# Performance work log

Hardware: AMD Instinct MI355X
Metric: run time of the kernel (lower is better)

## Reference

```python
import jax, jax.numpy as jnp
import numpy as np

B, S, D = 4, 2048, 1024
E, H = 1024, 16
HD = E // H
TEMPERATURE = 1.0


def setup_inputs() -> dict:
    key = jax.random.key(0)
    ks = jax.random.split(key, 6)
    x = jax.random.normal(ks[0], (B, S, D), dtype=jnp.float32)
    src_key_padding_mask = jnp.zeros((B, S), dtype=bool)  # unused by module
    matrix_mask = jax.random.normal(ks[1], (B, S, S), dtype=jnp.float32)
    # Xavier-uniform linear weights (torch Linear stores [out, in])
    lim_qkv = float(np.sqrt(6.0 / (D + 3 * E)))
    qkv_w = jax.random.uniform(ks[2], (3 * E, D), dtype=jnp.float32, minval=-lim_qkv, maxval=lim_qkv)
    qkv_b = jnp.zeros((3 * E,), dtype=jnp.float32)
    lim_o = float(np.sqrt(6.0 / (E + E)))
    o_w = jax.random.uniform(ks[3], (E, E), dtype=jnp.float32, minval=-lim_o, maxval=lim_o)
    o_b = jnp.zeros((E,), dtype=jnp.float32)
    return {"x": x, "src_key_padding_mask": src_key_padding_mask, "matrix_mask": matrix_mask,
            "qkv_w": qkv_w, "qkv_b": qkv_b, "o_w": o_w, "o_b": o_b}


def reference(x, src_key_padding_mask, matrix_mask, qkv_w, qkv_b, o_w, o_b):
    b, s, _ = x.shape
    qkv = x @ qkv_w.T + qkv_b                      # [B,S,3E]
    qkv = qkv.reshape(b, s, H, 3 * HD).transpose(0, 2, 1, 3)  # [B,H,S,3*HD]
    q, k, v = jnp.split(qkv, 3, axis=-1)           # each [B,H,S,HD]
    scale = 1.0 / np.sqrt(HD)
    logits = jnp.einsum('bhqd,bhkd->bhqk', q, k) * scale + matrix_mask[:, None, :, :]
    attn = jax.nn.softmax(logits / TEMPERATURE, axis=-1)  # [B,H,S,S]
    # dropout=0.0, eval mode -> no-op
    values = jnp.einsum('bhqk,bhkd->bhqd', attn, v)       # [B,H,S,HD]
    values = values.transpose(0, 2, 1, 3).reshape(b, s, E)
    o = values @ o_w.T + o_b                       # [B,S,E]
    attention_mean = jnp.mean(attn, axis=1)        # [B,S,S]
    return (o, attention_mean)
```

## Files before the change

### kernel.cpp

```cpp
#include <hip/hip_runtime.h>

#define B_ 4
#define S_ 2048
#define D_ 1024
#define E_ 1024
#define H_ 16
#define HD_ 64
#define SCALE 0.125f
#define LOG2E 1.44269504f
#define C1_ (SCALE * LOG2E)

typedef __bf16 bf16;
typedef __bf16 bf16x8 __attribute__((ext_vector_type(8)));
typedef __bf16 bf16x4 __attribute__((ext_vector_type(4)));
typedef float f32x4 __attribute__((ext_vector_type(4)));
typedef _Float16 f16x8 __attribute__((ext_vector_type(8)));
typedef _Float16 f16x4 __attribute__((ext_vector_type(4)));

static __device__ __forceinline__ f32x4 mfma16(bf16x8 a, bf16x8 b, f32x4 c) {
  return __builtin_amdgcn_mfma_f32_16x16x32_bf16(a, b, c, 0, 0, 0);
}

typedef __attribute__((address_space(3))) void lvoid;
typedef const __attribute__((address_space(1))) void gvoid;
static __device__ __forceinline__ void gload16(const void* g, void* l) {
  __builtin_amdgcn_global_load_lds((gvoid*)g, (lvoid*)l, 16, 0, 0);
}

static __device__ __forceinline__ float exp2a(float x) {
  float r;
  asm("v_exp_f32 %0, %1" : "=v"(r) : "v"(x));
  return r;
}

static __device__ __forceinline__ int rsw(int row) {
  return (row & 3) | (((row >> 3) & 1) << 2);
}

__global__ void k_cvt(const float* __restrict__ in, bf16* __restrict__ out, int n4) {
  int i = blockIdx.x * 256 + threadIdx.x;
  if (i >= n4) return;
  float4 v = reinterpret_cast<const float4*>(in)[i];
  bf16x4 o = { (bf16)v.x, (bf16)v.y, (bf16)v.z, (bf16)v.w };
  reinterpret_cast<bf16x4*>(out)[i] = o;
}

__global__ void k_cvt16(const float* __restrict__ in, _Float16* __restrict__ out, int n4) {
  int i = blockIdx.x * 256 + threadIdx.x;
  if (i >= n4) return;
  float4 v = reinterpret_cast<const float4*>(in)[i];
  f16x4 o = { (_Float16)(v.x * LOG2E), (_Float16)(v.y * LOG2E),
              (_Float16)(v.z * LOG2E), (_Float16)(v.w * LOG2E) };
  reinterpret_cast<f16x4*>(out)[i] = o;
}

__global__ __launch_bounds__(256) void k_qkv(const bf16* __restrict__ xb,
                                             const bf16* __restrict__ wb,
                                             const float* __restrict__ qkvb,
                                             bf16* __restrict__ Qw,
                                             bf16* __restrict__ Kw,
                                             bf16* __restrict__ Vtw) {
  __shared__ __align__(16) bf16 lA[128 * 32];
  __shared__ __align__(16) bf16 lB[128 * 32];
  const int tid = threadIdx.x, lane = tid & 63, wv = tid >> 6;
  const int u = lane >> 4, c = lane & 15;
  const int wr = wv >> 1, wc = wv & 1;
  const int m0 = blockIdx.y * 128;
  const int n0 = blockIdx.x * 128;
  const int sr = tid >> 2, sk = (tid & 3) * 8;
  const bf16* gA = xb + (size_t)(m0 + sr) * D_ + sk;
  const bf16* gB = wb + (size_t)(n0 + sr) * D_ + sk;
  bf16* lpA = lA + wv * 512;
  bf16* lpB = lB + wv * 512;
  f32x4 acc[4][4] = {};
  for (int k0 = 0; k0 < D_; k0 += 32) {
    gload16(gA + k0, lpA);
    gload16(gA + 64 * D_ + k0, lpA + 2048);
    gload16(gB + k0, lpB);
    gload16(gB + 64 * D_ + k0, lpB + 2048);
    __syncthreads();
    bf16x8 af[4], bfr[4];
#pragma unroll
    for (int m = 0; m < 4; ++m)
      af[m] = *(const bf16x8*)(lA + (wr * 64 + m * 16 + c) * 32 + u * 8);
#pragma unroll
    for (int n = 0; n < 4; ++n)
      bfr[n] = *(const bf16x8*)(lB + (wc * 64 + n * 16 + c) * 32 + u * 8);
#pragma unroll
    for (int m = 0; m < 4; ++m)
#pragma unroll
      for (int n = 0; n < 4; ++n)
        acc[m][n] = mfma16(af[m], bfr[n], acc[m][n]);
    __syncthreads();
  }
#pragma unroll
  for (int n = 0; n < 4; ++n) {
    int nn = n0 + wc * 64 + n * 16 + c;
    float bias = qkvb[nn];
    int h = nn / 192;
    int rem = nn - h * 192;
#pragma unroll
    for (int m = 0; m < 4; ++m) {
#pragma unroll
      for (int r = 0; r < 4; ++r) {
        int q = m0 + wr * 64 + m * 16 + 4 * u + r;
        int bb = q >> 11, s = q & 2047;
        bf16 v = (bf16)(acc[m][n][r] + bias);
        if (rem < 64)       Qw[((bb * H_ + h) * S_ + s) * HD_ + rem] = v;
        else if (rem < 128) Kw[((bb * H_ + h) * S_ + s) * HD_ + (rem - 64)] = v;
        else                Vtw[((bb * H_ + h) * HD_ + (rem - 128)) * S_ + s] = v;
      }
    }
  }
}

#define PV_TILE2(HC, HN, BS, KT, PF)                                          \
  {                                                                           \
    if (PF) {                                                                 \
      const bf16* ksrc = Kb + (size_t)((KT) + 1) * 64 * HD_;                  \
      gload16(ksrc + ksw1, (bf16*)kl[(BS) ^ 1] + wv * 512);                   \
      gload16(ksrc + ksw2, (bf16*)kl[(BS) ^ 1] + 2048 + wv * 512);            \
      const bf16* vsrc = Vb + (size_t)((KT) + 1) * 64;                        \
      gload16(vsrc + vsw1, (bf16*)vl[(BS) ^ 1] + wv * 512);                   \
      gload16(vsrc + vsw2, (bf16*)vl[(BS) ^ 1] + 2048 + wv * 512);            \
      __builtin_amdgcn_sched_barrier(0);                                      \
    }                                                                         \
    f32x4 sA[4], sB[4];                                                       \
    _Pragma("unroll")                                                         \
    for (int f = 0; f < 4; ++f) {                                             \
      int rk = 32 * (f & 1) + 8 * (c >> 2) + 4 * (f >> 1) + (c & 3);          \
      int sw = rsw(rk);                                                       \
      bf16x8 k0 = *(const bf16x8*)&kl[BS][rk * 64 + ((u ^ sw) * 8)];          \
      bf16x8 k1 = *(const bf16x8*)&kl[BS][rk * 64 + (((4 + u) ^ sw) * 8)];    \
      f32x4 a = {};                                                           \
      a = mfma16(k0, aqA0, a);                                                \
      a = mfma16(k1, aqA1, a);                                                \
      sA[f] = a;                                                              \
      f32x4 bb2 = {};                                                         \
      bb2 = mfma16(k0, aqB0, bb2);                                            \
      bb2 = mfma16(k1, aqB1, bb2);                                            \
      sB[f] = bb2;                                                            \
    }                                                                         \
    if (PF) {                                                                 \
      const _Float16* nA = bmrA + ((KT) + 1) * 64 + 8 * u;                    \
      const _Float16* nB = bmrB + ((KT) + 1) * 64 + 8 * u;                    \
      HN[0] = *(const f16x8*)(nA);                                            \
      HN[1] = *(const f16x8*)(nA + 32);                                       \
      HN[2] = *(const f16x8*)(nB);                                            \
      HN[3] = *(const f16x8*)(nB + 32);                                       \
    }                                                                         \
    float pA[16], pB[16];                                                     \
    _Pragma("unroll")                                                         \
    for (int f = 0; f < 4; ++f) {                                             \
      _Pragma("unroll")                                                       \
      for (int j = 0; j < 4; ++j) {                                           \
        float p = exp2a(sA[f][j] * C1_ + (float)HC[f & 1][4 * (f >> 1) + j]); \
        lsumA += p;                                                           \
        pA[f * 4 + j] = p;                                                    \
        float q2 = exp2a(sB[f][j] * C1_ +                                     \
                         (float)HC[2 + (f & 1)][4 * (f >> 1) + j]);           \
        lsumB += q2;                                                          \
        pB[f * 4 + j] = q2;                                                   \
      }                                                                       \
    }                                                                         \
    bf16x8 bpA0 = { (bf16)pA[0],  (bf16)pA[1],  (bf16)pA[2],  (bf16)pA[3],    \
                    (bf16)pA[8],  (bf16)pA[9],  (bf16)pA[10], (bf16)pA[11] }; \
    bf16x8 bpA1 = { (bf16)pA[4],  (bf16)pA[5],  (bf16)pA[6],  (bf16)pA[7],    \
                    (bf16)pA[12], (bf16)pA[13], (bf16)pA[14], (bf16)pA[15] }; \
    bf16x8 bpB0 = { (bf16)pB[0],  (bf16)pB[1],  (bf16)pB[2],  (bf16)pB[3],    \
                    (bf16)pB[8],  (bf16)pB[9],  (bf16)pB[10], (bf16)pB[11] }; \
    bf16x8 bpB1 = { (bf16)pB[4],  (bf16)pB[5],  (bf16)pB[6],  (bf16)pB[7],    \
                    (bf16)pB[12], (bf16)pB[13], (bf16)pB[14], (bf16)pB[15] }; \
    __builtin_amdgcn_s_setprio(1);                                            \
    _Pragma("unroll")                                                         \
    for (int g = 0; g < 4; ++g) {                                             \
      int rv = g * 16 + c;                                                    \
      int swv = rsw(rv);                                                      \
      bf16x8 v0 = *(const bf16x8*)&vl[BS][rv * 64 + ((u ^ swv) * 8)];         \
      bf16x8 v1 = *(const bf16x8*)&vl[BS][rv * 64 + (((4 + u) ^ swv) * 8)];   \
      accA[g] = mfma16(v0, bpA0, accA[g]);                                    \
      accA[g] = mfma16(v1, bpA1, accA[g]);                                    \
      accB[g] = mfma16(v0, bpB0, accB[g]);                                    \
      accB[g] = mfma16(v1, bpB1, accB[g]);                                    \
    }                                                                         \
    __builtin_amdgcn_s_setprio(0);                                            \
    asm volatile("s_waitcnt vmcnt(4) lgkmcnt(0)" ::: "memory");               \
    __builtin_amdgcn_s_barrier();                                             \
  }

__global__ __launch_bounds__(256) void k_pv(const bf16* __restrict__ Qw,
                                            const bf16* __restrict__ Kw,
                                            const bf16* __restrict__ Vtw,
                                            const _Float16* __restrict__ bmask,
                                            float* __restrict__ li_ws,
                                            bf16* __restrict__ valw) {
  __shared__ __align__(16) bf16 kl[2][64 * 64];
  __shared__ __align__(16) bf16 vl[2][64 * 64];
  const int tid = threadIdx.x, lane = tid & 63, wv = tid >> 6;
  const int u = lane >> 4, c = lane & 15;
  const int qt = blockIdx.x, h = blockIdx.y, b = blockIdx.z;
  const bf16* Qb = Qw + (size_t)(b * H_ + h) * S_ * HD_;
  const bf16* Kb = Kw + (size_t)(b * H_ + h) * S_ * HD_;
  const bf16* Vb = Vtw + (size_t)(b * H_ + h) * HD_ * S_;
  const int qrA = qt * 128 + wv * 32 + c;
  const int qrB = qrA + 16;
  bf16x8 aqA0 = *(const bf16x8*)(Qb + (size_t)qrA * HD_ + u * 8);
  bf16x8 aqA1 = *(const bf16x8*)(Qb + (size_t)qrA * HD_ + 32 + u * 8);
  bf16x8 aqB0 = *(const bf16x8*)(Qb + (size_t)qrB * HD_ + u * 8);
  bf16x8 aqB1 = *(const bf16x8*)(Qb + (size_t)qrB * HD_ + 32 + u * 8);
  const _Float16* bmrA = bmask + (size_t)b * S_ * S_ + (size_t)qrA * S_;
  const _Float16* bmrB = bmask + (size_t)b * S_ * S_ + (size_t)qrB * S_;
  const int r1 = tid >> 3, s1 = (tid & 7) ^ rsw(tid >> 3);
  const int g2i = tid + 256;
  const int r2 = g2i >> 3, s2 = (g2i & 7) ^ rsw(g2i >> 3);
  const int ksw1 = (r1 * 8 + s1) * 8, ksw2 = (r2 * 8 + s2) * 8;
  const int vsw1 = r1 * S_ + s1 * 8, vsw2 = r2 * S_ + s2 * 8;
  gload16(Kb + ksw1, (bf16*)kl[0] + wv * 512);
  gload16(Kb + ksw2, (bf16*)kl[0] + 2048 + wv * 512);
  gload16(Vb + vsw1, (bf16*)vl[0] + wv * 512);
  gload16(Vb + vsw2, (bf16*)vl[0] + 2048 + wv * 512);
  f16x8 hmA[4], hmB[4];
  hmA[0] = *(const f16x8*)(bmrA + 8 * u);
  hmA[1] = *(const f16x8*)(bmrA + 32 + 8 * u);
  hmA[2] = *(const f16x8*)(bmrB + 8 * u);
  hmA[3] = *(const f16x8*)(bmrB + 32 + 8 * u);
  f32x4 accA[4] = {}, accB[4] = {};
  float lsumA = 0.f, lsumB = 0.f;
  __syncthreads();
  for (int kt2 = 0; kt2 < 16; ++kt2) {
    PV_TILE2(hmA, hmB, 0, 2 * kt2, true);
    PV_TILE2(hmB, hmA, 1, 2 * kt2 + 1, (kt2 < 15));
  }
  lsumA += __shfl_xor(lsumA, 16, 64);
  lsumA += __shfl_xor(lsumA, 32, 64);
  lsumB += __shfl_xor(lsumB, 16, 64);
  lsumB += __shfl_xor(lsumB, 32, 64);
  float liA = 1.f / lsumA, liB = 1.f / lsumB;
  if (u == 0) {
    li_ws[(b * H_ + h) * S_ + qrA] = liA;
    li_ws[(b * H_ + h) * S_ + qrB] = liB;
  }
#pragma unroll
  for (int g = 0; g < 4; ++g) {
    bf16x4 pkA = { (bf16)(accA[g][0] * liA), (bf16)(accA[g][1] * liA),
                   (bf16)(accA[g][2] * liA), (bf16)(accA[g][3] * liA) };
    *(bf16x4*)(&valw[(size_t)(b * S_ + qrA) * E_ + h * HD_ + g * 16 + 4 * u]) = pkA;
    bf16x4 pkB = { (bf16)(accB[g][0] * liB), (bf16)(accB[g][1] * liB),
                   (bf16)(accB[g][2] * liB), (bf16)(accB[g][3] * liB) };
    *(bf16x4*)(&valw[(size_t)(b * S_ + qrB) * E_ + h * HD_ + g * 16 + 4 * u]) = pkB;
  }
}

#define MEAN_PHASE(QC0, QC1, QC2, QC3, QN0, QN1, QN2, QN3, BS, HH, PF)         \
  {                                                                            \
    if (PF) {                                                                  \
      const bf16* ksrc = Kw + (size_t)(bh0 + (HH) + 1) * S_ * HD_ +            \
                         (size_t)kt * 64 * HD_;                                \
      gload16(ksrc + sw1, (bf16*)kl2[(BS) ^ 1] + wv * 512);                    \
      gload16(ksrc + sw2, (bf16*)kl2[(BS) ^ 1] + 2048 + wv * 512);             \
      __builtin_amdgcn_sched_barrier(0);                                       \
    }                                                                          \
    bf16x8 kf[8];                                                              \
    _Pragma("unroll")                                                          \
    for (int f = 0; f < 4; ++f) {                                              \
      int row = f * 16 + c;                                                    \
      int sw = row & 7;                                                        \
      kf[2 * f]     = *(const bf16x8*)&kl2[BS][row * 64 + ((u ^ sw) * 8)];     \
      kf[2 * f + 1] = *(const bf16x8*)&kl2[BS][row * 64 + (((4 + u) ^ sw) * 8)];\
    }                                                                          \
    if (PF) {                                                                  \
      const bf16* Qn = Qw + (size_t)(bh0 + (HH) + 1) * S_ * HD_ +              \
                       (size_t)(qrow0 + c) * HD_ + u * 8;                      \
      QN0 = *(const bf16x8*)(Qn);                                              \
      QN1 = *(const bf16x8*)(Qn + 32);                                         \
      QN2 = *(const bf16x8*)(Qn + 64 * HD_);                                   \
      QN3 = *(const bf16x8*)(Qn + 64 * HD_ + 32);                              \
    }                                                                          \
    float llA = li_l[(HH) * 128 + wv * 16 + c];                                \
    float llB = li_l[(HH) * 128 + 64 + wv * 16 + c];                           \
    _Pragma("unroll")                                                          \
    for (int f = 0; f < 4; ++f) {                                              \
      f32x4 a = {};                                                            \
      a = mfma16(kf[2 * f], QC0, a);                                           \
      a = mfma16(kf[2 * f + 1], QC1, a);                                       \
      f32x4 bb = {};                                                           \
      bb = mfma16(kf[2 * f], QC2, bb);                                         \
      bb = mfma16(kf[2 * f + 1], QC3, bb);                                     \
      _Pragma("unroll")                                                        \
      for (int j = 0; j < 4; ++j) {                                            \
        maccA[f][j] += exp2a(a[j] * C1_ + (float)mhA[f][j]) * llA;             \
        maccB[f][j] += exp2a(bb[j] * C1_ + (float)mhB[f][j]) * llB;            \
      }                                                                        \
    }                                                                          \
    asm volatile("s_waitcnt vmcnt(4) lgkmcnt(0)" ::: "memory");                \
    __builtin_amdgcn_s_barrier();                                              \
  }

__global__ __launch_bounds__(256) void k_mean(const bf16* __restrict__ Qw,
                                              const bf16* __restrict__ Kw,
                                              const _Float16* __restrict__ bmask,
                                              const float* __restrict__ li_ws,
                                              float* __restrict__ mean_out) {
  __shared__ float li_l[H_ * 128];
  __shared__ __align__(16) bf16 kl2[2][64 * 64];
  const int tid = threadIdx.x, lane = tid & 63, wv = tid >> 6;
  const int u = lane >> 4, c = lane & 15;
  const int qt = blockIdx.x, kt = blockIdx.y, b = blockIdx.z;
  const int bh0 = b * H_;
  for (int i = tid; i < H_ * 128; i += 256) {
    int hh = i >> 7, q = i & 127;
    li_l[i] = li_ws[(bh0 + hh) * S_ + qt * 128 + q];
  }
  const int qrow0 = qt * 128 + wv * 16;
  f16x4 mhA[4], mhB[4];
  {
    const _Float16* bmpA = bmask + (size_t)b * S_ * S_ +
                           (size_t)(qrow0 + c) * S_ + (size_t)kt * 64 + 4 * u;
    const _Float16* bmpB = bmpA + (size_t)64 * S_;
#pragma unroll
    for (int f = 0; f < 4; ++f) {
      mhA[f] = *(const f16x4*)(bmpA + f * 16);
      mhB[f] = *(const f16x4*)(bmpB + f * 16);
    }
  }
  const int gg1 = wv * 64 + lane;
  const int gg2 = gg1 + 256;
  const int sw1 = (gg1 ^ ((gg1 >> 3) & 7)) * 8;
  const int sw2 = (gg2 ^ ((gg2 >> 3) & 7)) * 8;
  {
    const bf16* K0 = Kw + (size_t)bh0 * S_ * HD_ + (size_t)kt * 64 * HD_;
    gload16(K0 + sw1, (bf16*)kl2[0] + wv * 512);
    gload16(K0 + sw2, (bf16*)kl2[0] + 2048 + wv * 512);
  }
  bf16x8 qA0, qA1, qA2, qA3, qB0, qB1, qB2, qB3;
  {
    const bf16* Q0 = Qw + (size_t)bh0 * S_ * HD_ + (size_t)(qrow0 + c) * HD_ + u * 8;
    qA0 = *(const bf16x8*)Q0;
    qA1 = *(const bf16x8*)(Q0 + 32);
    qA2 = *(const bf16x8*)(Q0 + 64 * HD_);
    qA3 = *(const bf16x8*)(Q0 + 64 * HD_ + 32);
  }
  f32x4 maccA[4] = {}, maccB[4] = {};
  __syncthreads();
  for (int h2 = 0; h2 < 8; ++h2) {
    MEAN_PHASE(qA0, qA1, qA2, qA3, qB0, qB1, qB2, qB3, 0, 2 * h2, true);
    MEAN_PHASE(qB0, qB1, qB2, qB3, qA0, qA1, qA2, qA3, 1, 2 * h2 + 1, (h2 < 7));
  }
#pragma unroll
  for (int f = 0; f < 4; ++f) {
    f32x4 moA = maccA[f] * (1.f / 16.f);
    *(f32x4*)&mean_out[(size_t)b * S_ * S_ + (size_t)(qrow0 + c) * S_ +
                       (size_t)kt * 64 + f * 16 + 4 * u] = moA;
    f32x4 moB = maccB[f] * (1.f / 16.f);
    *(f32x4*)&mean_out[(size_t)b * S_ * S_ + (size_t)(qrow0 + 64 + c) * S_ +
                       (size_t)kt * 64 + f * 16 + 4 * u] = moB;
  }
}

__global__ __launch_bounds__(256) void k_oproj(const bf16* __restrict__ vb,
                                               const bf16* __restrict__ wo,
                                               const float* __restrict__ ob,
                                               float* __restrict__ out) {
  __shared__ __align__(16) bf16 lA[128 * 32];
  __shared__ __align__(16) bf16 lB[128 * 32];
  const int tid = threadIdx.x, lane = tid & 63, wv = tid >> 6;
  const int u = lane >> 4, c = lane & 15;
  const int wr = wv >> 1, wc = wv & 1;
  const int m0 = blockIdx.y * 128;
  const int n0 = blockIdx.x * 128;
  const int sr = tid >> 2, sk = (tid & 3) * 8;
  const bf16* gA = vb + (size_t)(m0 + sr) * E_ + sk;
  const bf16* gB = wo + (size_t)(n0 + sr) * E_ + sk;
  bf16* lpA = lA + wv * 512;
  bf16* lpB = lB + wv * 512;
  f32x4 acc[4][4] = {};
  for (int k0 = 0; k0 < E_; k0 += 32) {
    gload16(gA + k0, lpA);
    gload16(gA + 64 * E_ + k0, lpA + 2048);
    gload16(gB + k0, lpB);
    gload16(gB + 64 * E_ + k0, lpB + 2048);
    __syncthreads();
    bf16x8 af[4], bfr[4];
#pragma unroll
    for (int m = 0; m < 4; ++m)
      af[m] = *(const bf16x8*)(lA + (wr * 64 + m * 16 + c) * 32 + u * 8);
#pragma unroll
    for (int n = 0; n < 4; ++n)
      bfr[n] = *(const bf16x8*)(lB + (wc * 64 + n * 16 + c) * 32 + u * 8);
#pragma unroll
    for (int m = 0; m < 4; ++m)
#pragma unroll
      for (int n = 0; n < 4; ++n)
        acc[m][n] = mfma16(af[m], bfr[n], acc[m][n]);
    __syncthreads();
  }
#pragma unroll
  for (int n = 0; n < 4; ++n) {
    int nn = n0 + wc * 64 + n * 16 + c;
    float bias = ob[nn];
#pragma unroll
    for (int m = 0; m < 4; ++m) {
#pragma unroll
      for (int r = 0; r < 4; ++r) {
        int q = m0 + wr * 64 + m * 16 + 4 * u + r;
        out[(size_t)q * E_ + nn] = acc[m][n][r] + bias;
      }
    }
  }
}

extern "C" void kernel_launch(void* const* d_in, const int* in_sizes, int n_in,
                              void* d_out, int out_size, void* d_ws, size_t ws_size,
                              hipStream_t stream) {
  const float* x    = (const float*)d_in[0];
  const float* mmsk = (const float*)d_in[2];
  const float* qkvw = (const float*)d_in[3];
  const float* qkvb = (const float*)d_in[4];
  const float* ow   = (const float*)d_in[5];
  const float* ob   = (const float*)d_in[6];

  char* ws = (char*)d_ws;
  bf16* xb  = (bf16*)(ws);
  bf16* wb  = (bf16*)(ws + (16u << 20));
  bf16* owb = (bf16*)(ws + (22u << 20));
  bf16* Qw  = (bf16*)(ws + (24u << 20));
  bf16* Kw  = (bf16*)(ws + (40u << 20));
  bf16* Vtw = (bf16*)(ws + (56u << 20));
  float* li_ws = (float*)(ws + (16u << 20));
  bf16* values = xb;

  float* out_o    = (float*)d_out;
  float* out_mean = out_o + (size_t)B_ * S_ * E_;
  _Float16* bmask = (_Float16*)out_o;

  k_cvt<<<dim3(2097152 / 256), 256, 0, stream>>>(x, xb, 2097152);
  k_cvt<<<dim3(786432 / 256), 256, 0, stream>>>(qkvw, wb, 786432);
  k_cvt<<<dim3(262144 / 256), 256, 0, stream>>>(ow, owb, 262144);
  k_cvt16<<<dim3(4194304 / 256), 256, 0, stream>>>(mmsk, bmask, 4194304);
  k_qkv<<<dim3(24, 64), 256, 0, stream>>>(xb, wb, qkvb, Qw, Kw, Vtw);
  k_pv<<<dim3(16, 16, 4), 256, 0, stream>>>(Qw, Kw, Vtw, bmask, li_ws, values);
  k_mean<<<dim3(16, 32, 4), 256, 0, stream>>>(Qw, Kw, bmask, li_ws, out_mean);
  k_oproj<<<dim3(8, 64), 256, 0, stream>>>(values, owb, ob, out_o);
}
```

Baseline: 347.2 us.

## Simplify mean kernel to direct global loads and reorder PV prefetch

The mean kernel drops its LDS double-buffered K staging and shared li cache. Each wave now loads K, Q and li straight from global memory per head inside a plain loop, with no barriers. In the PV kernel, the async K/V prefetch for the next tile is moved after the QK MFMAs, and the hand-tuned partial waitcnt plus barrier is replaced by __syncthreads. This trades the explicit overlap of memory and compute for simpler code and fewer barriers, but risks exposed load latency and duplicated global K reads across waves.

```diff
diff --git a/kernel.cpp b/kernel.cpp
--- a/kernel.cpp
+++ b/kernel.cpp
@@ -116,15 +116,6 @@
 
 #define PV_TILE2(HC, HN, BS, KT, PF)                                          \
   {                                                                           \
-    if (PF) {                                                                 \
-      const bf16* ksrc = Kb + (size_t)((KT) + 1) * 64 * HD_;                  \
-      gload16(ksrc + ksw1, (bf16*)kl[(BS) ^ 1] + wv * 512);                   \
-      gload16(ksrc + ksw2, (bf16*)kl[(BS) ^ 1] + 2048 + wv * 512);            \
-      const bf16* vsrc = Vb + (size_t)((KT) + 1) * 64;                        \
-      gload16(vsrc + vsw1, (bf16*)vl[(BS) ^ 1] + wv * 512);                   \
-      gload16(vsrc + vsw2, (bf16*)vl[(BS) ^ 1] + 2048 + wv * 512);            \
-      __builtin_amdgcn_sched_barrier(0);                                      \
-    }                                                                         \
     f32x4 sA[4], sB[4];                                                       \
     _Pragma("unroll")                                                         \
     for (int f = 0; f < 4; ++f) {                                             \
@@ -142,6 +133,12 @@
       sB[f] = bb2;                                                            \
     }                                                                         \
     if (PF) {                                                                 \
+      const bf16* ksrc = Kb + (size_t)((KT) + 1) * 64 * HD_;                  \
+      gload16(ksrc + ksw1, (bf16*)kl[(BS) ^ 1] + wv * 512);                   \
+      gload16(ksrc + ksw2, (bf16*)kl[(BS) ^ 1] + 2048 + wv * 512);            \
+      const bf16* vsrc = Vb + (size_t)((KT) + 1) * 64;                        \
+      gload16(vsrc + vsw1, (bf16*)vl[(BS) ^ 1] + wv * 512);                   \
+      gload16(vsrc + vsw2, (bf16*)vl[(BS) ^ 1] + 2048 + wv * 512);            \
       const _Float16* nA = bmrA + ((KT) + 1) * 64 + 8 * u;                    \
       const _Float16* nB = bmrB + ((KT) + 1) * 64 + 8 * u;                    \
       HN[0] = *(const f16x8*)(nA);                                            \
@@ -184,8 +181,7 @@
       accB[g] = mfma16(v1, bpB1, accB[g]);                                    \
     }                                                                         \
     __builtin_amdgcn_s_setprio(0);                                            \
-    asm volatile("s_waitcnt vmcnt(4) lgkmcnt(0)" ::: "memory");               \
-    __builtin_amdgcn_s_barrier();                                             \
+    __syncthreads();                                                          \
   }
 
 __global__ __launch_bounds__(256) void k_pv(const bf16* __restrict__ Qw,
@@ -251,66 +247,15 @@
   }
 }
 
-#define MEAN_PHASE(QC0, QC1, QC2, QC3, QN0, QN1, QN2, QN3, BS, HH, PF)         \
-  {                                                                            \
-    if (PF) {                                                                  \
-      const bf16* ksrc = Kw + (size_t)(bh0 + (HH) + 1) * S_ * HD_ +            \
-                         (size_t)kt * 64 * HD_;                                \
-      gload16(ksrc + sw1, (bf16*)kl2[(BS) ^ 1] + wv * 512);                    \
-      gload16(ksrc + sw2, (bf16*)kl2[(BS) ^ 1] + 2048 + wv * 512);             \
-      __builtin_amdgcn_sched_barrier(0);                                       \
-    }                                                                          \
-    bf16x8 kf[8];                                                              \
-    _Pragma("unroll")                                                          \
-    for (int f = 0; f < 4; ++f) {                                              \
-      int row = f * 16 + c;                                                    \
-      int sw = row & 7;                                                        \
-      kf[2 * f]     = *(const bf16x8*)&kl2[BS][row * 64 + ((u ^ sw) * 8)];     \
-      kf[2 * f + 1] = *(const bf16x8*)&kl2[BS][row * 64 + (((4 + u) ^ sw) * 8)];\
-    }                                                                          \
-    if (PF) {                                                                  \
-      const bf16* Qn = Qw + (size_t)(bh0 + (HH) + 1) * S_ * HD_ +              \
-                       (size_t)(qrow0 + c) * HD_ + u * 8;                      \
-      QN0 = *(const bf16x8*)(Qn);                                              \
-      QN1 = *(const bf16x8*)(Qn + 32);                                         \
-      QN2 = *(const bf16x8*)(Qn + 64 * HD_);                                   \
-      QN3 = *(const bf16x8*)(Qn + 64 * HD_ + 32);                              \
-    }                                                                          \
-    float llA = li_l[(HH) * 128 + wv * 16 + c];                                \
-    float llB = li_l[(HH) * 128 + 64 + wv * 16 + c];                           \
-    _Pragma("unroll")                                                          \
-    for (int f = 0; f < 4; ++f) {                                              \
-      f32x4 a = {};                                                            \
-      a = mfma16(kf[2 * f], QC0, a);                                           \
-      a = mfma16(kf[2 * f + 1], QC1, a);                                       \
-      f32x4 bb = {};                                                           \
-      bb = mfma16(kf[2 * f], QC2, bb);                                         \
-      bb = mfma16(kf[2 * f + 1], QC3, bb);                                     \
-      _Pragma("unroll")                                                        \
-      for (int j = 0; j < 4; ++j) {                                            \
-        maccA[f][j] += exp2a(a[j] * C1_ + (float)mhA[f][j]) * llA;             \
-        maccB[f][j] += exp2a(bb[j] * C1_ + (float)mhB[f][j]) * llB;            \
-      }                                                                        \
-    }                                                                          \
-    asm volatile("s_waitcnt vmcnt(4) lgkmcnt(0)" ::: "memory");                \
-    __builtin_amdgcn_s_barrier();                                              \
-  }
-
 __global__ __launch_bounds__(256) void k_mean(const bf16* __restrict__ Qw,
                                               const bf16* __restrict__ Kw,
                                               const _Float16* __restrict__ bmask,
                                               const float* __restrict__ li_ws,
                                               float* __restrict__ mean_out) {
-  __shared__ float li_l[H_ * 128];
-  __shared__ __align__(16) bf16 kl2[2][64 * 64];
   const int tid = threadIdx.x, lane = tid & 63, wv = tid >> 6;
   const int u = lane >> 4, c = lane & 15;
   const int qt = blockIdx.x, kt = blockIdx.y, b = blockIdx.z;
   const int bh0 = b * H_;
-  for (int i = tid; i < H_ * 128; i += 256) {
-    int hh = i >> 7, q = i & 127;
-    li_l[i] = li_ws[(bh0 + hh) * S_ + qt * 128 + q];
-  }
   const int qrow0 = qt * 128 + wv * 16;
   f16x4 mhA[4], mhB[4];
   {
@@ -323,28 +268,39 @@
       mhB[f] = *(const f16x4*)(bmpB + f * 16);
     }
   }
-  const int gg1 = wv * 64 + lane;
-  const int gg2 = gg1 + 256;
-  const int sw1 = (gg1 ^ ((gg1 >> 3) & 7)) * 8;
-  const int sw2 = (gg2 ^ ((gg2 >> 3) & 7)) * 8;
-  {
-    const bf16* K0 = Kw + (size_t)bh0 * S_ * HD_ + (size_t)kt * 64 * HD_;
-    gload16(K0 + sw1, (bf16*)kl2[0] + wv * 512);
-    gload16(K0 + sw2, (bf16*)kl2[0] + 2048 + wv * 512);
-  }
-  bf16x8 qA0, qA1, qA2, qA3, qB0, qB1, qB2, qB3;
-  {
-    const bf16* Q0 = Qw + (size_t)bh0 * S_ * HD_ + (size_t)(qrow0 + c) * HD_ + u * 8;
-    qA0 = *(const bf16x8*)Q0;
-    qA1 = *(const bf16x8*)(Q0 + 32);
-    qA2 = *(const bf16x8*)(Q0 + 64 * HD_);
-    qA3 = *(const bf16x8*)(Q0 + 64 * HD_ + 32);
-  }
   f32x4 maccA[4] = {}, maccB[4] = {};
-  __syncthreads();
-  for (int h2 = 0; h2 < 8; ++h2) {
-    MEAN_PHASE(qA0, qA1, qA2, qA3, qB0, qB1, qB2, qB3, 0, 2 * h2, true);
-    MEAN_PHASE(qB0, qB1, qB2, qB3, qA0, qA1, qA2, qA3, 1, 2 * h2 + 1, (h2 < 7));
+#pragma unroll 2
+  for (int h = 0; h < H_; ++h) {
+    const bf16* Kh = Kw + (size_t)(bh0 + h) * S_ * HD_ + (size_t)kt * 64 * HD_;
+    bf16x8 kf[8];
+#pragma unroll
+    for (int f = 0; f < 4; ++f) {
+      kf[2 * f]     = *(const bf16x8*)(Kh + (f * 16 + c) * HD_ + u * 8);
+      kf[2 * f + 1] = *(const bf16x8*)(Kh + (f * 16 + c) * HD_ + 32 + u * 8);
+    }
+    const bf16* Qh = Qw + (size_t)(bh0 + h) * S_ * HD_ +
+                     (size_t)(qrow0 + c) * HD_ + u * 8;
+    bf16x8 q0 = *(const bf16x8*)Qh;
+    bf16x8 q1 = *(const bf16x8*)(Qh + 32);
+    bf16x8 q2 = *(const bf16x8*)(Qh + 64 * HD_);
+    bf16x8 q3 = *(const bf16x8*)(Qh + 64 * HD_ + 32);
+    const float* lp = li_ws + (size_t)(bh0 + h) * S_ + qt * 128 + wv * 16 + c;
+    float llA = lp[0];
+    float llB = lp[64];
+#pragma unroll
+    for (int f = 0; f < 4; ++f) {
+      f32x4 a = {};
+      a = mfma16(kf[2 * f], q0, a);
+      a = mfma16(kf[2 * f + 1], q1, a);
+      f32x4 bb = {};
+      bb = mfma16(kf[2 * f], q2, bb);
+      bb = mfma16(kf[2 * f + 1], q3, bb);
+#pragma unroll
+      for (int j = 0; j < 4; ++j) {
+        maccA[f][j] += exp2a(a[j] * C1_ + (float)mhA[f][j]) * llA;
+        maccB[f][j] += exp2a(bb[j] * C1_ + (float)mhB[f][j]) * llB;
+      }
+    }
   }
 #pragma unroll
   for (int f = 0; f < 4; ++f) {
```

New measurement: 429.3 us. +23.6%, slower.
